# Kernel tuning notes

Hardware: AMD Instinct MI355X
Metric: run time of the kernel (lower is better)

Reference implementation:

```python
import jax, jax.numpy as jnp
import numpy as np

EMBED_DIM = 4096
LOW_RANK = 512
BATCH = 8192
K_SEL = 128


def setup_inputs() -> dict:
    key = jax.random.key(0)
    k1, k2, k3, k4 = jax.random.split(key, 4)
    base = jax.random.normal(k1, (BATCH, EMBED_DIM), dtype=jnp.float32)
    source = jax.random.normal(k2, (BATCH, EMBED_DIM), dtype=jnp.float32)
    # fast path: only subspaces[0] is used (all examples share the same index set)
    row = jax.random.randint(k3, (1, K_SEL), 0, LOW_RANK)
    subspaces = jnp.broadcast_to(row, (BATCH, K_SEL)).astype(jnp.int64)
    # orthogonal (column-orthonormal) rotation weight, as produced by
    # torch.nn.utils.parametrizations.orthogonal on [embed_dim, low_rank]
    W, _ = jnp.linalg.qr(jax.random.normal(k4, (EMBED_DIM, LOW_RANK), dtype=jnp.float32))
    return {"base": base, "source": source, "subspaces": subspaces, "W": W}


def reference(base, source, subspaces, W):
    # rotated_base / rotated_source: [B, r]
    # diff in rotated space, gather selected subspace columns, project back.
    sel = subspaces[0]                      # [k] shared index set (fast path)
    diff = (source - base) @ W              # [B, r]
    diff_sel = diff[:, sel]                 # [B, k]
    W_sel = W[:, sel]                       # [d, k]
    out = base + diff_sel @ W_sel.T         # [B, d]
    return out.astype(base.dtype)
```

## Files before the change

### kernel.cpp

```cpp
#include <hip/hip_runtime.h>
#include <hip/hip_bf16.h>

typedef __attribute__((ext_vector_type(4))) float  f32x4;
typedef __attribute__((ext_vector_type(8))) short  short8;

#define EMBED 4096
#define LR    512
#define KSEL  128
#define BATCH 8192

__device__ __forceinline__ short f2bf(float x) {
  union { float f; unsigned u; } c; c.f = x;
  unsigned r = c.u + 0x7FFFu + ((c.u >> 16) & 1u);
  return (short)(r >> 16);
}

__global__ __launch_bounds__(256) void pack_w_kernel(
    const float* __restrict__ W, const int* __restrict__ sel,
    short* __restrict__ Wp, short* __restrict__ Wtp) {
  int idx = blockIdx.x * 256 + threadIdx.x;
  int e = idx >> 7;
  int c = idx & 127;
  int r = sel[c];
  short v = f2bf(W[e * LR + r]);
  Wp [(((e >> 3) << 7) + c) * 8 + (e & 7)] = v;
  Wtp[(((c >> 3) << 12) + e) * 8 + (c & 7)] = v;
}

__global__ __launch_bounds__(512) void gemm1_kernel(
    const float* __restrict__ base, const float* __restrict__ src,
    const short* __restrict__ Wp, short* __restrict__ Tp) {
  __shared__ f32x4 red[8 * 8 * 64];
  const int t  = threadIdx.x;
  const int w  = t >> 6, l = t & 63;
  const int lr = l & 15, lg = l >> 4;
  const int row0 = blockIdx.x * 16;
  const int k0 = w * 512;

  const float* bp = base + (size_t)(row0 + lr) * EMBED + k0 + lg * 8;
  const float* sp = src  + (size_t)(row0 + lr) * EMBED + k0 + lg * 8;

  f32x4 acc[8];
  #pragma unroll
  for (int nf = 0; nf < 8; ++nf) acc[nf] = (f32x4){0.f, 0.f, 0.f, 0.f};

  #pragma unroll 4
  for (int it = 0; it < 16; ++it) {
    const int kb = it * 32;
    f32x4 b0 = *(const f32x4*)(bp + kb);
    f32x4 b1 = *(const f32x4*)(bp + kb + 4);
    f32x4 s0 = *(const f32x4*)(sp + kb);
    f32x4 s1 = *(const f32x4*)(sp + kb + 4);
    short8 a;
    #pragma unroll
    for (int j = 0; j < 4; ++j) {
      a[j]     = f2bf(s0[j] - b0[j]);
      a[4 + j] = f2bf(s1[j] - b1[j]);
    }
    const int e = k0 + kb + lg * 8;
    const short8* wrow = (const short8*)Wp + ((e >> 3) << 7);
    #pragma unroll
    for (int nf = 0; nf < 8; ++nf)
      acc[nf] = __builtin_amdgcn_mfma_f32_16x16x32_bf16(a, wrow[nf * 16 + lr], acc[nf], 0, 0, 0);
  }

  #pragma unroll
  for (int nf = 0; nf < 8; ++nf) red[(w << 9) + (nf << 6) + l] = acc[nf];
  __syncthreads();
  {
    const int rl = t & 63, rnf = t >> 6;
    f32x4 s = red[(rnf << 6) + rl];
    #pragma unroll
    for (int w2 = 1; w2 < 8; ++w2) s += red[(w2 << 9) + (rnf << 6) + rl];
    const int kk = rnf * 16 + (rl & 15);
    short* dst = Tp + (size_t)(((kk >> 3) << 13) + row0 + ((rl >> 4) << 2)) * 8 + (kk & 7);
    #pragma unroll
    for (int r = 0; r < 4; ++r) dst[r * 8] = f2bf(s[r]);
  }
}

__global__ __launch_bounds__(256) void gemm2_kernel(
    const float* __restrict__ base, const short* __restrict__ Tp,
    const short* __restrict__ Wtp, float* __restrict__ out) {
  const int t  = threadIdx.x;
  const int w  = t >> 6, l = t & 63;
  const int lr = l & 15, lg = l >> 4;
  const int mt = blockIdx.x >> 4, nt = blockIdx.x & 15;
  const int row0 = mt * 64;
  const int col0 = nt * 256 + w * 64;

  short8 afr[4][4];
  #pragma unroll
  for (int m = 0; m < 4; ++m)
    #pragma unroll
    for (int ks = 0; ks < 4; ++ks)
      afr[m][ks] = *(const short8*)(Tp + (size_t)(((ks * 4 + lg) << 13) + row0 + m * 16 + lr) * 8);

  f32x4 acc[4][4];
  #pragma unroll
  for (int m = 0; m < 4; ++m)
    #pragma unroll
    for (int nf = 0; nf < 4; ++nf) acc[m][nf] = (f32x4){0.f, 0.f, 0.f, 0.f};

  #pragma unroll
  for (int nf = 0; nf < 4; ++nf) {
    short8 bfr[4];
    #pragma unroll
    for (int ks = 0; ks < 4; ++ks)
      bfr[ks] = *(const short8*)(Wtp + (size_t)(((ks * 4 + lg) << 12) + col0 + nf * 16 + lr) * 8);
    #pragma unroll
    for (int m = 0; m < 4; ++m)
      #pragma unroll
      for (int ks = 0; ks < 4; ++ks)
        acc[m][nf] = __builtin_amdgcn_mfma_f32_16x16x32_bf16(afr[m][ks], bfr[ks], acc[m][nf], 0, 0, 0);
  }

  #pragma unroll
  for (int m = 0; m < 4; ++m)
    #pragma unroll
    for (int r = 0; r < 4; ++r) {
      const size_t row = row0 + m * 16 + lg * 4 + r;
      #pragma unroll
      for (int nf = 0; nf < 4; ++nf) {
        const size_t o = row * EMBED + col0 + nf * 16 + lr;
        out[o] = base[o] + acc[m][nf][r];
      }
    }
}

extern "C" void kernel_launch(void* const* d_in, const int* in_sizes, int n_in,
                              void* d_out, int out_size, void* d_ws, size_t ws_size,
                              hipStream_t stream) {
  const float* base = (const float*)d_in[0];
  const float* src  = (const float*)d_in[1];
  const int*   sub  = (const int*)d_in[2];
  const float* W    = (const float*)d_in[3];
  float* out = (float*)d_out;

  short* Wp  = (short*)d_ws;
  short* Wtp = Wp  + EMBED * KSEL;
  short* Tp  = Wtp + EMBED * KSEL;

  pack_w_kernel<<<EMBED * KSEL / 256, 256, 0, stream>>>(W, sub, Wp, Wtp);
  gemm1_kernel<<<BATCH / 16, 512, 0, stream>>>(base, src, Wp, Tp);
  gemm2_kernel<<<(BATCH / 64) * 16, 256, 0, stream>>>(base, Tp, Wtp, out);
}
```

Measured before the change: 140.2 us.

## Stage gemm1 activations through LDS with async double-buffered global_load_lds

Gemm1 now stages 16-row tiles of base and source into a double-buffered shared-memory region using direct global-to-LDS loads. The row chunks are XOR-swizzled to avoid bank conflicts, and the next stage is prefetched while the current one is computed. Work is split so each wave owns half of K and two of the eight N fragments, not one K slice with all eight, which shrinks the cross-wave reduction from 8 to 2 partials. The aim is better latency hiding and more coalesced streaming of the fp32 inputs, at the cost of 64KB of LDS per block (lower occupancy) and a barrier every stage.

After: 139.1 us. About the same (-0.8%).

```diff
diff --git a/kernel.cpp b/kernel.cpp
--- a/kernel.cpp
+++ b/kernel.cpp
@@ -3,6 +3,7 @@
 
 typedef __attribute__((ext_vector_type(4))) float  f32x4;
 typedef __attribute__((ext_vector_type(8))) short  short8;
+typedef unsigned int u32;
 
 #define EMBED 4096
 #define LR    512
@@ -13,6 +14,11 @@
   union { float f; unsigned u; } c; c.f = x;
   unsigned r = c.u + 0x7FFFu + ((c.u >> 16) & 1u);
   return (short)(r >> 16);
+}
+
+__device__ __forceinline__ void gload16(const void* g, void* l) {
+  __builtin_amdgcn_global_load_lds((const __attribute__((address_space(1))) u32*)g,
+                                   (__attribute__((address_space(3))) u32*)l, 16, 0, 0);
 }
 
 __global__ __launch_bounds__(256) void pack_w_kernel(
@@ -30,52 +36,74 @@
 __global__ __launch_bounds__(512) void gemm1_kernel(
     const float* __restrict__ base, const float* __restrict__ src,
     const short* __restrict__ Wp, short* __restrict__ Tp) {
-  __shared__ f32x4 red[8 * 8 * 64];
+  __shared__ char smem[65536];
   const int t  = threadIdx.x;
   const int w  = t >> 6, l = t & 63;
   const int lr = l & 15, lg = l >> 4;
   const int row0 = blockIdx.x * 16;
-  const int k0 = w * 512;
+  const int kh  = w >> 2;
+  const int nf0 = (w & 3) * 2;
 
-  const float* bp = base + (size_t)(row0 + lr) * EMBED + k0 + lg * 8;
-  const float* sp = src  + (size_t)(row0 + lr) * EMBED + k0 + lg * 8;
+  const int srow = t >> 5;
+  const int schg = ((t & 31) ^ (srow & 7)) << 2;
+  const size_t soff = (size_t)(row0 + srow) * EMBED + schg;
+  const float* g_b0 = base + soff;
+  const float* g_b1 = base + soff + 2048;
+  const float* g_s0 = src  + soff;
+  const float* g_s1 = src  + soff + 2048;
 
-  f32x4 acc[8];
-  #pragma unroll
-  for (int nf = 0; nf < 8; ++nf) acc[nf] = (f32x4){0.f, 0.f, 0.f, 0.f};
+  f32x4 acc0 = {0.f, 0.f, 0.f, 0.f}, acc1 = {0.f, 0.f, 0.f, 0.f};
 
-  #pragma unroll 4
-  for (int it = 0; it < 16; ++it) {
-    const int kb = it * 32;
-    f32x4 b0 = *(const f32x4*)(bp + kb);
-    f32x4 b1 = *(const f32x4*)(bp + kb + 4);
-    f32x4 s0 = *(const f32x4*)(sp + kb);
-    f32x4 s1 = *(const f32x4*)(sp + kb + 4);
-    short8 a;
+  #define STAGE(s, b) do {                                            \
+    char* d_ = smem + (b) * 32768 + t * 16;                           \
+    gload16(g_b0 + (s) * 128, d_);                                    \
+    gload16(g_b1 + (s) * 128, d_ + 8192);                             \
+    gload16(g_s0 + (s) * 128, d_ + 16384);                            \
+    gload16(g_s1 + (s) * 128, d_ + 24576);                            \
+  } while (0)
+
+  STAGE(0, 0);
+  int b = 0;
+  for (int s = 0; s < 16; ++s) {
+    __syncthreads();
+    if (s + 1 < 16) STAGE(s + 1, b ^ 1);
+    const char* tb = smem + b * 32768 + kh * 8192 + lr * 512;
+    const int kgb = kh * 2048 + s * 128;
     #pragma unroll
-    for (int j = 0; j < 4; ++j) {
-      a[j]     = f2bf(s0[j] - b0[j]);
-      a[4 + j] = f2bf(s1[j] - b1[j]);
+    for (int ksub = 0; ksub < 4; ++ksub) {
+      const int kin = ksub * 32 + lg * 8;
+      const int c0 = (kin >> 2) ^ (lr & 7);
+      const int c1 = ((kin >> 2) + 1) ^ (lr & 7);
+      f32x4 b0 = *(const f32x4*)(tb + c0 * 16);
+      f32x4 b1 = *(const f32x4*)(tb + c1 * 16);
+      f32x4 s0 = *(const f32x4*)(tb + 16384 + c0 * 16);
+      f32x4 s1 = *(const f32x4*)(tb + 16384 + c1 * 16);
+      short8 a;
+      #pragma unroll
+      for (int j = 0; j < 4; ++j) {
+        a[j]     = f2bf(s0[j] - b0[j]);
+        a[4 + j] = f2bf(s1[j] - b1[j]);
+      }
+      const short8* wrow = (const short8*)Wp + (((kgb + kin) >> 3) << 7);
+      acc0 = __builtin_amdgcn_mfma_f32_16x16x32_bf16(a, wrow[nf0 * 16 + lr],       acc0, 0, 0, 0);
+      acc1 = __builtin_amdgcn_mfma_f32_16x16x32_bf16(a, wrow[(nf0 + 1) * 16 + lr], acc1, 0, 0, 0);
     }
-    const int e = k0 + kb + lg * 8;
-    const short8* wrow = (const short8*)Wp + ((e >> 3) << 7);
-    #pragma unroll
-    for (int nf = 0; nf < 8; ++nf)
-      acc[nf] = __builtin_amdgcn_mfma_f32_16x16x32_bf16(a, wrow[nf * 16 + lr], acc[nf], 0, 0, 0);
+    b ^= 1;
   }
+  #undef STAGE
 
-  #pragma unroll
-  for (int nf = 0; nf < 8; ++nf) red[(w << 9) + (nf << 6) + l] = acc[nf];
+  __syncthreads();
+  f32x4* red = (f32x4*)smem;
+  red[w * 128 + l]      = acc0;
+  red[w * 128 + 64 + l] = acc1;
   __syncthreads();
   {
-    const int rl = t & 63, rnf = t >> 6;
-    f32x4 s = red[(rnf << 6) + rl];
+    const int w03 = t >> 7, nf = (t >> 6) & 1, l2 = t & 63;
+    f32x4 sum = red[w03 * 128 + nf * 64 + l2] + red[(w03 + 4) * 128 + nf * 64 + l2];
+    const int kk = w03 * 32 + nf * 16 + (l2 & 15);
+    short* dst = Tp + (size_t)(((kk >> 3) << 13) + row0 + ((l2 >> 4) << 2)) * 8 + (kk & 7);
     #pragma unroll
-    for (int w2 = 1; w2 < 8; ++w2) s += red[(w2 << 9) + (rnf << 6) + rl];
-    const int kk = rnf * 16 + (rl & 15);
-    short* dst = Tp + (size_t)(((kk >> 3) << 13) + row0 + ((rl >> 4) << 2)) * 8 + (kk & 7);
-    #pragma unroll
-    for (int r = 0; r < 4; ++r) dst[r * 8] = f2bf(s[r]);
+    for (int r = 0; r < 4; ++r) dst[r * 8] = f2bf(sum[r]);
   }
 }
 
```

## Stage bf16 diff tile in LDS and split gemm1 over output columns

Applied to the files above, without the earlier changes.

gemm1 now converts the block's 16 rows of (source - base) to bf16 once and stores them in a 128KB swizzled LDS buffer. Each wave then owns 16 output columns across the full K dimension instead of a K-slice of all columns, which removes the cross-wave LDS reduction. W fragments are prefetched one step ahead from global memory. The large LDS allocation limits occupancy to one block per CU, and global loads are now issued as a separate phase before compute rather than interleaved with MFMAs.

Result: faster. 125.2 us (-10.7%).

```diff
diff --git a/kernel.cpp b/kernel.cpp
--- a/kernel.cpp
+++ b/kernel.cpp
@@ -27,56 +27,74 @@
   Wtp[(((c >> 3) << 12) + e) * 8 + (c & 7)] = v;
 }
 
-__global__ __launch_bounds__(512) void gemm1_kernel(
+__global__ __launch_bounds__(512, 1) void gemm1_kernel(
     const float* __restrict__ base, const float* __restrict__ src,
     const short* __restrict__ Wp, short* __restrict__ Tp) {
-  __shared__ f32x4 red[8 * 8 * 64];
+  __shared__ __align__(16) char Alds[131072];
   const int t  = threadIdx.x;
   const int w  = t >> 6, l = t & 63;
   const int lr = l & 15, lg = l >> 4;
   const int row0 = blockIdx.x * 16;
-  const int k0 = w * 512;
 
-  const float* bp = base + (size_t)(row0 + lr) * EMBED + k0 + lg * 8;
-  const float* sp = src  + (size_t)(row0 + lr) * EMBED + k0 + lg * 8;
+  #pragma unroll
+  for (int rr = 0; rr < 2; ++rr) {
+    const int r = 2 * w + rr;
+    const float* bp = base + (size_t)(row0 + r) * EMBED;
+    const float* sp = src  + (size_t)(row0 + r) * EMBED;
+    char* arow = Alds + r * 8192;
+    const int rsw = r & 7;
+    #pragma unroll
+    for (int g = 0; g < 4; ++g) {
+      const int k0 = g * 1024 + l * 4;
+      f32x4 vb0 = *(const f32x4*)(bp + k0);
+      f32x4 vb1 = *(const f32x4*)(bp + k0 + 256);
+      f32x4 vb2 = *(const f32x4*)(bp + k0 + 512);
+      f32x4 vb3 = *(const f32x4*)(bp + k0 + 768);
+      f32x4 vs0 = *(const f32x4*)(sp + k0);
+      f32x4 vs1 = *(const f32x4*)(sp + k0 + 256);
+      f32x4 vs2 = *(const f32x4*)(sp + k0 + 512);
+      f32x4 vs3 = *(const f32x4*)(sp + k0 + 768);
+      asm volatile("" :: "v"(vb0[0]), "v"(vb1[0]), "v"(vb2[0]), "v"(vb3[0]),
+                         "v"(vs0[0]), "v"(vs1[0]), "v"(vs2[0]), "v"(vs3[0]));
+      #pragma unroll
+      for (int q = 0; q < 4; ++q) {
+        f32x4 vb = q == 0 ? vb0 : q == 1 ? vb1 : q == 2 ? vb2 : vb3;
+        f32x4 vs = q == 0 ? vs0 : q == 1 ? vs1 : q == 2 ? vs2 : vs3;
+        union { unsigned u[2]; __hip_bfloat162 h[2]; } uo;
+        uo.h[0] = __float22bfloat162_rn(make_float2(vs[0] - vb[0], vs[1] - vb[1]));
+        uo.h[1] = __float22bfloat162_rn(make_float2(vs[2] - vb[2], vs[3] - vb[3]));
+        const int c = (g * 4 + q) * 32 + (l >> 1);
+        char* dst = arow + ((c ^ rsw) << 4) + (l & 1) * 8;
+        *(unsigned*)dst = uo.u[0];
+        *(unsigned*)(dst + 4) = uo.u[1];
+      }
+    }
+  }
+  __syncthreads();
 
-  f32x4 acc[8];
-  #pragma unroll
-  for (int nf = 0; nf < 8; ++nf) acc[nf] = (f32x4){0.f, 0.f, 0.f, 0.f};
+  const short8* wq = (const short8*)Wp + w * 16 + lr;
+  const char* arow = Alds + lr * 8192;
+  const int rsw = lr & 7;
 
+  f32x4 acc = {0.f, 0.f, 0.f, 0.f};
+  short8 bA = wq[(size_t)(0 * 8 + 0 + lg) * 128];
+  short8 bB = wq[(size_t)(0 * 8 + 4 + lg) * 128];
   #pragma unroll 4
-  for (int it = 0; it < 16; ++it) {
-    const int kb = it * 32;
-    f32x4 b0 = *(const f32x4*)(bp + kb);
-    f32x4 b1 = *(const f32x4*)(bp + kb + 4);
-    f32x4 s0 = *(const f32x4*)(sp + kb);
-    f32x4 s1 = *(const f32x4*)(sp + kb + 4);
-    short8 a;
-    #pragma unroll
-    for (int j = 0; j < 4; ++j) {
-      a[j]     = f2bf(s0[j] - b0[j]);
-      a[4 + j] = f2bf(s1[j] - b1[j]);
-    }
-    const int e = k0 + kb + lg * 8;
-    const short8* wrow = (const short8*)Wp + ((e >> 3) << 7);
-    #pragma unroll
-    for (int nf = 0; nf < 8; ++nf)
-      acc[nf] = __builtin_amdgcn_mfma_f32_16x16x32_bf16(a, wrow[nf * 16 + lr], acc[nf], 0, 0, 0);
+  for (int s = 0; s < 64; ++s) {
+    const int sn = (s < 63) ? s + 1 : 63;
+    short8 nA = wq[(size_t)(sn * 8 + lg) * 128];
+    short8 nB = wq[(size_t)(sn * 8 + 4 + lg) * 128];
+    short8 a0 = *(const short8*)(arow + (((s * 8 + lg)     ^ rsw) << 4));
+    short8 a1 = *(const short8*)(arow + (((s * 8 + 4 + lg) ^ rsw) << 4));
+    acc = __builtin_amdgcn_mfma_f32_16x16x32_bf16(a0, bA, acc, 0, 0, 0);
+    acc = __builtin_amdgcn_mfma_f32_16x16x32_bf16(a1, bB, acc, 0, 0, 0);
+    bA = nA; bB = nB;
   }
 
+  const int kk = w * 16 + lr;
+  short* dst = Tp + (size_t)(((kk >> 3) << 13) + row0 + (lg << 2)) * 8 + (kk & 7);
   #pragma unroll
-  for (int nf = 0; nf < 8; ++nf) red[(w << 9) + (nf << 6) + l] = acc[nf];
-  __syncthreads();
-  {
-    const int rl = t & 63, rnf = t >> 6;
-    f32x4 s = red[(rnf << 6) + rl];
-    #pragma unroll
-    for (int w2 = 1; w2 < 8; ++w2) s += red[(w2 << 9) + (rnf << 6) + rl];
-    const int kk = rnf * 16 + (rl & 15);
-    short* dst = Tp + (size_t)(((kk >> 3) << 13) + row0 + ((rl >> 4) << 2)) * 8 + (kk & 7);
-    #pragma unroll
-    for (int r = 0; r < 4; ++r) dst[r * 8] = f2bf(s[r]);
-  }
+  for (int r = 0; r < 4; ++r) dst[r * 8] = f2bf(acc[r]);
 }
 
 __global__ __launch_bounds__(256) void gemm2_kernel(
```
